# Optimization experiments

Measured on AMD Instinct MI355X. Metric: run time of the kernel, lower is better.

Reference implementation:

```python
import jax, jax.numpy as jnp
import numpy as np

BLOCK_SIZE = 1024
OUTLIER_SIGMA = 3.0
OUT_FEATURES = 11008
IN_FEATURES = 4096
TOKENS = 64


def _quantize_mixed_np(W):
    """Faithful numpy port of quantize_mixed (BLOCK_SIZE divides numel exactly here)."""
    flat = W.astype(np.float32).reshape(-1)
    nb = flat.size // BLOCK_SIZE
    blocks = flat.reshape(nb, BLOCK_SIZE)
    mu = blocks.mean(axis=1, keepdims=True)
    sig = np.maximum(blocks.std(axis=1, ddof=1, keepdims=True), 1e-8)  # torch.std is unbiased
    outlier = np.abs(blocks - mu) > OUTLIER_SIGMA * sig
    abs_max = np.maximum(np.abs(np.where(outlier, 0.0, blocks)).max(axis=1), 1e-8)
    scales = (abs_max / 127.0).astype(np.float16)
    q = np.clip(np.round(blocks / abs_max[:, None] * 127.0), -127, 127).astype(np.int8)
    all_pos = np.arange(nb, dtype=np.int64)[:, None] * BLOCK_SIZE + np.arange(BLOCK_SIZE, dtype=np.int64)[None, :]
    int8_data = q[~outlier]                      # row-major == torch order
    fp16_data = blocks[outlier].astype(np.float16)
    int8_pos = all_pos[~outlier].astype(np.int32)
    fp16_pos = all_pos[outlier].astype(np.int32)
    block_idx = np.nonzero(~outlier)[0].astype(np.int32)  # block index per int8 value
    return int8_data, fp16_data, scales, int8_pos, fp16_pos, block_idx


def setup_inputs() -> dict:
    key = jax.random.key(0)
    k_x, k_b = jax.random.split(key)
    rng = np.random.default_rng(0)
    W = (rng.standard_normal((OUT_FEATURES, IN_FEATURES)) * 0.02).astype(np.float32)
    int8_data, fp16_data, scales, int8_pos, fp16_pos, block_idx = _quantize_mixed_np(W)
    x = jax.random.normal(k_x, (TOKENS, IN_FEATURES), dtype=jnp.float16)
    bias = jax.random.normal(k_b, (OUT_FEATURES,), dtype=jnp.float16) * jnp.float16(0.02)
    return {
        "x": x,
        "int8_data": jnp.asarray(int8_data),
        "fp16_data": jnp.asarray(fp16_data),
        "scales": jnp.asarray(scales),
        "bias": bias,
        "int8_pos": jnp.asarray(int8_pos),
        "fp16_pos": jnp.asarray(fp16_pos),
        "block_idx": jnp.asarray(block_idx),
    }


def reference(x, int8_data, fp16_data, scales, bias, int8_pos, fp16_pos, block_idx):
    out_features = bias.shape[0]
    in_features = x.shape[1]
    numel = out_features * in_features  # divisible by BLOCK_SIZE for these dims
    # dequantize_mixed: scatter fp16 outliers and dequantized int8 values into flat fp16 buffer
    flat = jnp.zeros((numel,), dtype=jnp.float16)
    flat = flat.at[fp16_pos].set(fp16_data)
    flat = flat.at[int8_pos].set(int8_data.astype(jnp.float16) * scales[block_idx])
    W = flat.reshape(out_features, in_features)
    # F.linear(x, W, bias) in fp16
    return jnp.dot(x.astype(jnp.float16), W.T) + bias
```

## Files before the change

### kernel.cpp

```cpp
#include <hip/hip_runtime.h>
#include <hip/hip_fp16.h>

#define TOK   64
#define INF   4096
#define OUTF  11008
#define NUMEL (OUTF * INF)
#define NSLC  (NUMEL / 64)
#define NBLK  (OUTF / 16)
#define KSPL  8
#define OUTN  (TOK * OUTF)

typedef __attribute__((ext_vector_type(8))) _Float16 half8;
typedef __attribute__((ext_vector_type(4))) _Float16 half4;
typedef __attribute__((ext_vector_type(4))) float floatx4;
typedef __attribute__((ext_vector_type(4), aligned(4))) int int4u;
typedef __attribute__((ext_vector_type(4))) int int4a;

__global__ __launch_bounds__(256) void precompute_kernel(
    const float* __restrict__ x, const int* __restrict__ fppos, int nf,
    _Float16* __restrict__ x16, int* __restrict__ meta) {
  const int t = blockIdx.x * 256 + threadIdx.x;
  if (t < (TOK * INF) / 4) {
    const floatx4 f = *(const floatx4*)&x[t * 4];
    half4 h;
    h[0] = (_Float16)f[0]; h[1] = (_Float16)f[1];
    h[2] = (_Float16)f[2]; h[3] = (_Float16)f[3];
    *(half4*)&x16[t * 4] = h;
  }
  if (t < NSLC) {
    const int target = t << 6;
    int lo = 0, hi = nf;
    while (lo < hi) {
      const int mid = (lo + hi) >> 1;
      if (fppos[mid] < target) lo = mid + 1; else hi = mid;
    }
    unsigned long long mask = 0ull;
    int j = lo;
    while (j < nf) {
      const int d = fppos[j] - target;
      if (d >= 64) break;
      mask |= 1ull << d;
      ++j;
    }
    int4a mv;
    mv[0] = lo;
    mv[1] = (int)(unsigned)(mask & 0xffffffffu);
    mv[2] = (int)(unsigned)(mask >> 32);
    mv[3] = 0;
    *(int4a*)&meta[t * 4] = mv;
  }
}

__device__ __forceinline__ void meta_window1(const int p0, const int4a mv,
                                             int& i0, unsigned& m8) {
  const unsigned mlo = (unsigned)mv[1];
  const unsigned mhi = (unsigned)mv[2];
  const int off = p0 & 63;
  m8 = 0xffu & (off < 32 ? (mlo >> off) : (mhi >> (off - 32)));
  const unsigned bl = (off >= 32) ? mlo : (mlo & ((1u << off) - 1u));
  const unsigned bh = (off >= 32) ? (mhi & ((1u << (off - 32)) - 1u)) : 0u;
  i0 = p0 - mv[0] - (__popc(bl) + __popc(bh));
}

__device__ __forceinline__ half8 finish_slot(
    const unsigned m8, const int i0, const int p0, const float s,
    const int (&l)[8], const int* __restrict__ i8,
    const float* __restrict__ fpdat, const int n8) {
  const int f = (int)m8;
  float ov[8];
#pragma unroll
  for (int e = 0; e < 8; ++e) ov[e] = 0.f;
  if (f) {
    int fi = p0 - i0;
#pragma unroll
    for (int e = 0; e < 8; ++e) {
      if ((f >> e) & 1) { ov[e] = fpdat[fi]; ++fi; }
    }
  }

  half8 oh;
  if (i0 + 8 <= n8) {
    if (f == 0) {
#pragma unroll
      for (int e = 0; e < 8; ++e) oh[e] = (_Float16)((float)l[e] * s);
    } else {
      int q = 0;
#pragma unroll
      for (int e = 0; e < 8; ++e) {
        const int flg = (f >> e) & 1;
        int lv = l[0];
#pragma unroll
        for (int qq = 1; qq < 8; ++qq) lv = (q == qq) ? l[qq] : lv;
        oh[e] = flg ? (_Float16)ov[e] : (_Float16)((float)lv * s);
        q += 1 - flg;
      }
    }
  } else {
    int c = 0;
    const int m = n8 - 1;
#pragma unroll
    for (int e = 0; e < 8; ++e) {
      const int flg = (f >> e) & 1;
      int idx = i0 + e - c;
      idx = idx < 0 ? 0 : (idx > m ? m : idx);
      oh[e] = flg ? (_Float16)ov[e] : (_Float16)((float)i8[idx] * s);
      c += flg;
    }
  }
  return oh;
}

struct Pre {
  int la[8], lb[8];
  int i0a, i0b;
  unsigned m8a, m8b;
  float va0, va1, vb0, vb1;
};

__global__ __launch_bounds__(256, 4) void gemm_fused(
    const _Float16* __restrict__ x16, const int* __restrict__ i8,
    const float* __restrict__ fpdat, const float* __restrict__ scales,
    const int* __restrict__ meta, float* __restrict__ part,
    const int n8, const int nf) {
  __shared__ float red[4 * 64 * 16];

  const int tid  = threadIdx.x;
  const int wave = tid >> 6;
  const int lane = tid & 63;
  const int quad = lane >> 4;
  const int ln   = lane & 15;
  const int nt   = blockIdx.x >> 3;
  const int kq   = blockIdx.x & 7;
  const int n0   = nt << 4;
  const int kbas = kq * 512 + wave * 128;
  const int qoff = quad * 8;

  const int prow  = n0 + ln;
  const int pbase = prow * INF + kbas;
  const float s   = scales[prow * 4 + (kq >> 1)];

#define ISSUE(BNK, CC, MV)                                                   \
  do {                                                                       \
    const int p0a_ = pbase + (CC) * 64 + qoff;                               \
    meta_window1(p0a_, (MV), BNK.i0a, BNK.m8a);                              \
    meta_window1(p0a_ + 32, (MV), BNK.i0b, BNK.m8b);                         \
    if (BNK.i0a + 8 <= n8) {                                                 \
      *(int4u*)&BNK.la[0] = *(const int4u*)&i8[BNK.i0a];                     \
      *(int4u*)&BNK.la[4] = *(const int4u*)&i8[BNK.i0a + 4];                 \
    }                                                                        \
    if (BNK.i0b + 8 <= n8) {                                                 \
      *(int4u*)&BNK.lb[0] = *(const int4u*)&i8[BNK.i0b];                     \
      *(int4u*)&BNK.lb[4] = *(const int4u*)&i8[BNK.i0b + 4];                 \
    }                                                                        \
      \
    {                                                                        \
      int fia_ = p0a_ - BNK.i0a;                                             \
      fia_ = fia_ < nf - 1 ? fia_ : nf - 1;                                  \
      BNK.va0 = fpdat[fia_];                                                 \
      BNK.va1 = fpdat[fia_ + 1 < nf ? fia_ + 1 : nf - 1];                    \
      int fib_ = p0a_ + 32 - BNK.i0b;                                        \
      fib_ = fib_ < nf - 1 ? fib_ : nf - 1;                                  \
      BNK.vb0 = fpdat[fib_];                                                 \
      BNK.vb1 = fpdat[fib_ + 1 < nf ? fib_ + 1 : nf - 1];                    \
    }                                                                        \
  } while (0)

#define FSLOT(OH, LARR, M8, I0, V0, V1)                                      \
  do {                                                                       \
    const int f_ = (int)(M8);                                                \
    if ((I0) + 8 <= n8) {                                                    \
      if (f_ == 0) {                                                         \
        _Pragma("unroll")                                                    \
        for (int e = 0; e < 8; ++e) OH[e] = (_Float16)((float)LARR[e] * s);  \
      } else {                                                               \
        int q_ = 0;                                                          \
        _Pragma("unroll")                                                    \
        for (int e = 0; e < 8; ++e) {                                        \
          const int flg = (f_ >> e) & 1;                                     \
          const int rank = __popc(f_ & ((1 << e) - 1));                      \
          const float fv = (rank == 0) ? (V0) : (V1);                        \
          int lv = LARR[0];                                                  \
          _Pragma("unroll")                                                  \
          for (int qq = 1; qq < 8; ++qq) lv = (q_ == qq) ? LARR[qq] : lv;    \
          OH[e] = flg ? (_Float16)fv : (_Float16)((float)lv * s);            \
          q_ += 1 - flg;                                                     \
        }                                                                    \
      }                                                                      \
    } else {                                                                 \
      int c_ = 0;                                                            \
      const int m_ = n8 - 1;                                                 \
      _Pragma("unroll")                                                      \
      for (int e = 0; e < 8; ++e) {                                          \
        const int flg = (f_ >> e) & 1;                                       \
        const int rank = __popc(f_ & ((1 << e) - 1));                        \
        const float fv = (rank == 0) ? (V0) : (V1);                          \
        int idx = (I0) + e - c_;                                             \
        idx = idx < 0 ? 0 : (idx > m_ ? m_ : idx);                           \
        OH[e] = flg ? (_Float16)fv : (_Float16)((float)i8[idx] * s);         \
        c_ += flg;                                                           \
      }                                                                      \
    }                                                                        \
  } while (0)

#define LOADA(CC)                                                            \
  do {                                                                       \
    const _Float16* ap_ = &x16[ln * INF + kbas + (CC) * 64 + qoff];          \
    A0 = *(const half8*)&ap_[0];                                             \
    A1 = *(const half8*)&ap_[16 * INF];                                      \
    A2 = *(const half8*)&ap_[32 * INF];                                      \
    A3 = *(const half8*)&ap_[48 * INF];                                      \
    A4 = *(const half8*)&ap_[32];                                            \
    A5 = *(const half8*)&ap_[16 * INF + 32];                                 \
    A6 = *(const half8*)&ap_[32 * INF + 32];                                 \
    A7 = *(const half8*)&ap_[48 * INF + 32];                                 \
  } while (0)

#define FIN_MFMA(BNK, CC)                                                    \
  do {                                                                       \
    const int p0a_ = pbase + (CC) * 64 + qoff;                               \
    half8 b0, b1;                                                            \
    FSLOT(b0, BNK.la, BNK.m8a, BNK.i0a, BNK.va0, BNK.va1);                   \
    FSLOT(b1, BNK.lb, BNK.m8b, BNK.i0b, BNK.vb0, BNK.vb1);                   \
    if (__any(__popc((int)BNK.m8a) > 2 || __popc((int)BNK.m8b) > 2)) {       \
      if (__popc((int)BNK.m8a) > 2)                                          \
        b0 = finish_slot(BNK.m8a, BNK.i0a, p0a_, s, BNK.la, i8, fpdat, n8);  \
      if (__popc((int)BNK.m8b) > 2)                                          \
        b1 = finish_slot(BNK.m8b, BNK.i0b, p0a_ + 32, s, BNK.lb,             \
                         i8, fpdat, n8);                                     \
    }                                                                        \
    acc0 = __builtin_amdgcn_mfma_f32_16x16x32_f16(A0, b0, acc0, 0, 0, 0);    \
    acc1 = __builtin_amdgcn_mfma_f32_16x16x32_f16(A1, b0, acc1, 0, 0, 0);    \
    acc2 = __builtin_amdgcn_mfma_f32_16x16x32_f16(A2, b0, acc2, 0, 0, 0);    \
    acc3 = __builtin_amdgcn_mfma_f32_16x16x32_f16(A3, b0, acc3, 0, 0, 0);    \
    acc0 = __builtin_amdgcn_mfma_f32_16x16x32_f16(A4, b1, acc0, 0, 0, 0);    \
    acc1 = __builtin_amdgcn_mfma_f32_16x16x32_f16(A5, b1, acc1, 0, 0, 0);    \
    acc2 = __builtin_amdgcn_mfma_f32_16x16x32_f16(A6, b1, acc2, 0, 0, 0);    \
    acc3 = __builtin_amdgcn_mfma_f32_16x16x32_f16(A7, b1, acc3, 0, 0, 0);    \
  } while (0)

  const int4a mz0 = *(const int4a*)&meta[(pbase >> 6) * 4];
  const int4a mz1 = *(const int4a*)&meta[((pbase + 64) >> 6) * 4];
  half8 A0, A1, A2, A3, A4, A5, A6, A7;
  LOADA(0);
  Pre pA, pB;
  ISSUE(pA, 0, mz0);
  ISSUE(pB, 1, mz1);

  floatx4 acc0 = {0,0,0,0}, acc1 = {0,0,0,0}, acc2 = {0,0,0,0}, acc3 = {0,0,0,0};

  FIN_MFMA(pA, 0);
  LOADA(1);
  FIN_MFMA(pB, 1);

#undef ISSUE
#undef FSLOT
#undef LOADA
#undef FIN_MFMA

  const int mb = quad * 4;
#pragma unroll
  for (int i = 0; i < 4; ++i) red[wave * 1024 + (mb + i)      * 16 + ln] = acc0[i];
#pragma unroll
  for (int i = 0; i < 4; ++i) red[wave * 1024 + (16 + mb + i) * 16 + ln] = acc1[i];
#pragma unroll
  for (int i = 0; i < 4; ++i) red[wave * 1024 + (32 + mb + i) * 16 + ln] = acc2[i];
#pragma unroll
  for (int i = 0; i < 4; ++i) red[wave * 1024 + (48 + mb + i) * 16 + ln] = acc3[i];
  __syncthreads();

  float* pp = &part[(size_t)kq * OUTN];
#pragma unroll
  for (int c2 = 0; c2 < 4; ++c2) {
    const int cell = tid + c2 * 256;
    const int mm = cell >> 4, nn = cell & 15;
    pp[mm * OUTF + n0 + nn] =
        red[cell] + red[1024 + cell] + red[2048 + cell] + red[3072 + cell];
  }
}

__global__ __launch_bounds__(256) void reduce_kernel(
    const float* __restrict__ part, const float* __restrict__ bias,
    float* __restrict__ out) {
  const int t  = blockIdx.x * 256 + threadIdx.x;
  const int i4 = t * 4;
  floatx4 a = *(const floatx4*)&part[i4];
#pragma unroll
  for (int k = 1; k < KSPL; ++k) {
    const floatx4 b = *(const floatx4*)&part[(size_t)k * OUTN + i4];
    a[0] += b[0]; a[1] += b[1]; a[2] += b[2]; a[3] += b[3];
  }
  const int nn = i4 % OUTF;
  const floatx4 bb = *(const floatx4*)&bias[nn];
  a[0] += bb[0]; a[1] += bb[1]; a[2] += bb[2]; a[3] += bb[3];
  *(floatx4*)&out[i4] = a;
}

extern "C" void kernel_launch(void* const* d_in, const int* in_sizes, int n_in,
                              void* d_out, int out_size, void* d_ws,
                              size_t ws_size, hipStream_t stream) {
  const float* x      = (const float*)d_in[0];
  const int*   i8     = (const int*)d_in[1];
  const float* fpdat  = (const float*)d_in[2];
  const float* scales = (const float*)d_in[3];
  const float* bias   = (const float*)d_in[4];
  const int*   fppos  = (const int*)d_in[6];

  char* wsp = (char*)d_ws;
  _Float16* x16  = (_Float16*)wsp;
  int*      meta = (int*)(wsp + (size_t)TOK * INF * sizeof(_Float16));
  float*    part = (float*)(wsp + (size_t)TOK * INF * sizeof(_Float16)
                                + (size_t)NSLC * 16);
  float*    out  = (float*)d_out;

  const int n8 = in_sizes[1];
  const int nf = in_sizes[2];

  precompute_kernel<<<NSLC / 256, 256, 0, stream>>>(x, fppos, nf, x16, meta);
  gemm_fused<<<NBLK * KSPL, 256, 0, stream>>>(x16, i8, fpdat, scales, meta,
                                              part, n8, nf);
  reduce_kernel<<<OUTN / (4 * 256), 256, 0, stream>>>(part, bias, out);
}
```

Baseline: 435.2 us.

## Double split-K factor so each wave dequantizes and multiplies one chunk

```diff
diff --git a/kernel.cpp b/kernel.cpp
--- a/kernel.cpp
+++ b/kernel.cpp
@@ -7,7 +7,7 @@
 #define NUMEL (OUTF * INF)
 #define NSLC  (NUMEL / 64)
 #define NBLK  (OUTF / 16)
-#define KSPL  8
+#define KSPL  16
 #define OUTN  (TOK * OUTF)
 
 typedef __attribute__((ext_vector_type(8))) _Float16 half8;
@@ -110,13 +110,6 @@
   return oh;
 }
 
-struct Pre {
-  int la[8], lb[8];
-  int i0a, i0b;
-  unsigned m8a, m8b;
-  float va0, va1, vb0, vb1;
-};
-
 __global__ __launch_bounds__(256, 4) void gemm_fused(
     const _Float16* __restrict__ x16, const int* __restrict__ i8,
     const float* __restrict__ fpdat, const float* __restrict__ scales,
@@ -129,41 +122,53 @@
   const int lane = tid & 63;
   const int quad = lane >> 4;
   const int ln   = lane & 15;
-  const int nt   = blockIdx.x >> 3;
-  const int kq   = blockIdx.x & 7;
+  const int nt   = blockIdx.x >> 4;
+  const int kq   = blockIdx.x & 15;
   const int n0   = nt << 4;
-  const int kbas = kq * 512 + wave * 128;
+  const int kbas = kq * 256 + wave * 64;
   const int qoff = quad * 8;
 
   const int prow  = n0 + ln;
   const int pbase = prow * INF + kbas;
-  const float s   = scales[prow * 4 + (kq >> 1)];
-
-#define ISSUE(BNK, CC, MV)                                                   \
-  do {                                                                       \
-    const int p0a_ = pbase + (CC) * 64 + qoff;                               \
-    meta_window1(p0a_, (MV), BNK.i0a, BNK.m8a);                              \
-    meta_window1(p0a_ + 32, (MV), BNK.i0b, BNK.m8b);                         \
-    if (BNK.i0a + 8 <= n8) {                                                 \
-      *(int4u*)&BNK.la[0] = *(const int4u*)&i8[BNK.i0a];                     \
-      *(int4u*)&BNK.la[4] = *(const int4u*)&i8[BNK.i0a + 4];                 \
-    }                                                                        \
-    if (BNK.i0b + 8 <= n8) {                                                 \
-      *(int4u*)&BNK.lb[0] = *(const int4u*)&i8[BNK.i0b];                     \
-      *(int4u*)&BNK.lb[4] = *(const int4u*)&i8[BNK.i0b + 4];                 \
-    }                                                                        \
-      \
-    {                                                                        \
-      int fia_ = p0a_ - BNK.i0a;                                             \
-      fia_ = fia_ < nf - 1 ? fia_ : nf - 1;                                  \
-      BNK.va0 = fpdat[fia_];                                                 \
-      BNK.va1 = fpdat[fia_ + 1 < nf ? fia_ + 1 : nf - 1];                    \
-      int fib_ = p0a_ + 32 - BNK.i0b;                                        \
-      fib_ = fib_ < nf - 1 ? fib_ : nf - 1;                                  \
-      BNK.vb0 = fpdat[fib_];                                                 \
-      BNK.vb1 = fpdat[fib_ + 1 < nf ? fib_ + 1 : nf - 1];                    \
-    }                                                                        \
-  } while (0)
+  const float s   = scales[prow * 4 + (kbas >> 10)];
+
+  const int4a mz = *(const int4a*)&meta[(pbase >> 6) * 4];
+  const _Float16* ap = &x16[ln * INF + kbas + qoff];
+  const half8 A0 = *(const half8*)&ap[0];
+  const half8 A1 = *(const half8*)&ap[16 * INF];
+  const half8 A2 = *(const half8*)&ap[32 * INF];
+  const half8 A3 = *(const half8*)&ap[48 * INF];
+  const half8 A4 = *(const half8*)&ap[32];
+  const half8 A5 = *(const half8*)&ap[16 * INF + 32];
+  const half8 A6 = *(const half8*)&ap[32 * INF + 32];
+  const half8 A7 = *(const half8*)&ap[48 * INF + 32];
+
+  const int p0a = pbase + qoff;
+  int i0a, i0b;
+  unsigned m8a, m8b;
+  meta_window1(p0a, mz, i0a, m8a);
+  meta_window1(p0a + 32, mz, i0b, m8b);
+
+  int la[8], lb[8];
+  if (i0a + 8 <= n8) {
+    *(int4u*)&la[0] = *(const int4u*)&i8[i0a];
+    *(int4u*)&la[4] = *(const int4u*)&i8[i0a + 4];
+  }
+  if (i0b + 8 <= n8) {
+    *(int4u*)&lb[0] = *(const int4u*)&i8[i0b];
+    *(int4u*)&lb[4] = *(const int4u*)&i8[i0b + 4];
+  }
+  float va0, va1, vb0, vb1;
+  {
+    int fia = p0a - i0a;
+    fia = fia < nf - 1 ? fia : nf - 1;
+    va0 = fpdat[fia];
+    va1 = fpdat[fia + 1 < nf ? fia + 1 : nf - 1];
+    int fib = p0a + 32 - i0b;
+    fib = fib < nf - 1 ? fib : nf - 1;
+    vb0 = fpdat[fib];
+    vb1 = fpdat[fib + 1 < nf ? fib + 1 : nf - 1];
+  }
 
 #define FSLOT(OH, LARR, M8, I0, V0, V1)                                      \
   do {                                                                       \
@@ -202,60 +207,26 @@
     }                                                                        \
   } while (0)
 
-#define LOADA(CC)                                                            \
-  do {                                                                       \
-    const _Float16* ap_ = &x16[ln * INF + kbas + (CC) * 64 + qoff];          \
-    A0 = *(const half8*)&ap_[0];                                             \
-    A1 = *(const half8*)&ap_[16 * INF];                                      \
-    A2 = *(const half8*)&ap_[32 * INF];                                      \
-    A3 = *(const half8*)&ap_[48 * INF];                                      \
-    A4 = *(const half8*)&ap_[32];                                            \
-    A5 = *(const half8*)&ap_[16 * INF + 32];                                 \
-    A6 = *(const half8*)&ap_[32 * INF + 32];                                 \
-    A7 = *(const half8*)&ap_[48 * INF + 32];                                 \
-  } while (0)
-
-#define FIN_MFMA(BNK, CC)                                                    \
-  do {                                                                       \
-    const int p0a_ = pbase + (CC) * 64 + qoff;                               \
-    half8 b0, b1;                                                            \
-    FSLOT(b0, BNK.la, BNK.m8a, BNK.i0a, BNK.va0, BNK.va1);                   \
-    FSLOT(b1, BNK.lb, BNK.m8b, BNK.i0b, BNK.vb0, BNK.vb1);                   \
-    if (__any(__popc((int)BNK.m8a) > 2 || __popc((int)BNK.m8b) > 2)) {       \
-      if (__popc((int)BNK.m8a) > 2)                                          \
-        b0 = finish_slot(BNK.m8a, BNK.i0a, p0a_, s, BNK.la, i8, fpdat, n8);  \
-      if (__popc((int)BNK.m8b) > 2)                                          \
-        b1 = finish_slot(BNK.m8b, BNK.i0b, p0a_ + 32, s, BNK.lb,             \
-                         i8, fpdat, n8);                                     \
-    }                                                                        \
-    acc0 = __builtin_amdgcn_mfma_f32_16x16x32_f16(A0, b0, acc0, 0, 0, 0);    \
-    acc1 = __builtin_amdgcn_mfma_f32_16x16x32_f16(A1, b0, acc1, 0, 0, 0);    \
-    acc2 = __builtin_amdgcn_mfma_f32_16x16x32_f16(A2, b0, acc2, 0, 0, 0);    \
-    acc3 = __builtin_amdgcn_mfma_f32_16x16x32_f16(A3, b0, acc3, 0, 0, 0);    \
-    acc0 = __builtin_amdgcn_mfma_f32_16x16x32_f16(A4, b1, acc0, 0, 0, 0);    \
-    acc1 = __builtin_amdgcn_mfma_f32_16x16x32_f16(A5, b1, acc1, 0, 0, 0);    \
-    acc2 = __builtin_amdgcn_mfma_f32_16x16x32_f16(A6, b1, acc2, 0, 0, 0);    \
-    acc3 = __builtin_amdgcn_mfma_f32_16x16x32_f16(A7, b1, acc3, 0, 0, 0);    \
-  } while (0)
-
-  const int4a mz0 = *(const int4a*)&meta[(pbase >> 6) * 4];
-  const int4a mz1 = *(const int4a*)&meta[((pbase + 64) >> 6) * 4];
-  half8 A0, A1, A2, A3, A4, A5, A6, A7;
-  LOADA(0);
-  Pre pA, pB;
-  ISSUE(pA, 0, mz0);
-  ISSUE(pB, 1, mz1);
+  half8 b0, b1;
+  FSLOT(b0, la, m8a, i0a, va0, va1);
+  FSLOT(b1, lb, m8b, i0b, vb0, vb1);
+  if (__any(__popc((int)m8a) > 2 || __popc((int)m8b) > 2)) {
+    if (__popc((int)m8a) > 2)
+      b0 = finish_slot(m8a, i0a, p0a, s, la, i8, fpdat, n8);
+    if (__popc((int)m8b) > 2)
+      b1 = finish_slot(m8b, i0b, p0a + 32, s, lb, i8, fpdat, n8);
+  }
+#undef FSLOT
 
   floatx4 acc0 = {0,0,0,0}, acc1 = {0,0,0,0}, acc2 = {0,0,0,0}, acc3 = {0,0,0,0};
-
-  FIN_MFMA(pA, 0);
-  LOADA(1);
-  FIN_MFMA(pB, 1);
-
-#undef ISSUE
-#undef FSLOT
-#undef LOADA
-#undef FIN_MFMA
+  acc0 = __builtin_amdgcn_mfma_f32_16x16x32_f16(A0, b0, acc0, 0, 0, 0);
+  acc1 = __builtin_amdgcn_mfma_f32_16x16x32_f16(A1, b0, acc1, 0, 0, 0);
+  acc2 = __builtin_amdgcn_mfma_f32_16x16x32_f16(A2, b0, acc2, 0, 0, 0);
+  acc3 = __builtin_amdgcn_mfma_f32_16x16x32_f16(A3, b0, acc3, 0, 0, 0);
+  acc0 = __builtin_amdgcn_mfma_f32_16x16x32_f16(A4, b1, acc0, 0, 0, 0);
+  acc1 = __builtin_amdgcn_mfma_f32_16x16x32_f16(A5, b1, acc1, 0, 0, 0);
+  acc2 = __builtin_amdgcn_mfma_f32_16x16x32_f16(A6, b1, acc2, 0, 0, 0);
+  acc3 = __builtin_amdgcn_mfma_f32_16x16x32_f16(A7, b1, acc3, 0, 0, 0);
 
   const int mb = quad * 4;
 #pragma unroll
```

Result: no change. 442.6 us (+1.7%).
